# Performance work log

Measured on AMD Instinct MI355X. Metric: run time of the kernel, lower is better.

## Reference

```python
import jax, jax.numpy as jnp
import numpy as np

B, S, E, H = 4, 1024, 512, 16

def setup_inputs() -> dict:
    key = jax.random.key(0)
    ks = jax.random.split(key, 6)
    return {
        "x": jax.random.normal(ks[0], (B, S, E), dtype=jnp.float32),
        "Wq": jax.random.normal(ks[1], (E, E), dtype=jnp.float32) * (E ** -0.5),
        "Wk": jax.random.normal(ks[2], (E, E), dtype=jnp.float32) * (E ** -0.5),
        "Wv": jax.random.normal(ks[3], (E, E), dtype=jnp.float32) * (E ** -0.5),
        "W1": jax.random.normal(ks[4], (H, 2 * E), dtype=jnp.float32) * ((2 * E) ** -0.5),
        "b1": jnp.zeros((H,), dtype=jnp.float32),
        "W2": jax.random.normal(ks[5], (1, H), dtype=jnp.float32) * (H ** -0.5),
        "b2": jnp.zeros((1,), dtype=jnp.float32),
    }

def reference(x, Wq, Wk, Wv, W1, b1, W2, b2):
    embed_dim = x.shape[-1]
    # nn.Linear: y = x @ W.T
    Q = jnp.einsum('bse,oe->bso', x, Wq)
    K = jnp.einsum('bse,oe->bso', x, Wk)
    V = jnp.einsum('bse,oe->bso', x, Wv)
    scores = jnp.einsum('bqe,bke->bqk', Q, K) / jnp.sqrt(jnp.float32(embed_dim))
    # Estimator on concat([Q_i, K_j]): split W1 so we never materialize the
    # [B,S,S,2E] pair tensor; concat(q,k)@W1.T == q@W1[:, :E].T + k@W1[:, E:].T
    W1q, W1k = W1[:, :embed_dim], W1[:, embed_dim:]
    hq = jnp.einsum('bqe,he->bqh', Q, W1q)          # [B,S,H]
    hk = jnp.einsum('bke,he->bkh', K, W1k)          # [B,S,H]
    hid = jnp.tanh(hq[:, :, None, :] + hk[:, None, :, :] + b1)  # [B,S,S,H]
    est = jnp.einsum('bqkh,h->bqk', hid, W2[0]) + b2[0]
    attn = jax.nn.softmax(scores + est, axis=-1)
    return jnp.einsum('bqk,bke->bqe', attn, V)
```

## Files before the change

### kernel.cpp

```cpp
#include <hip/hip_runtime.h>
#include <hip/hip_fp16.h>


#define DEVI __device__ __forceinline__

typedef _Float16 half8 __attribute__((ext_vector_type(8)));
typedef _Float16 half4v __attribute__((ext_vector_type(4)));
typedef float f32x4 __attribute__((ext_vector_type(4)));

DEVI void gload16(const void* g, void* l) {
  __builtin_amdgcn_global_load_lds(
      (const __attribute__((address_space(1))) void*)g,
      (__attribute__((address_space(3))) void*)l, 16, 0, 0);
}

DEVI half8 cvt8(float4 a, float4 b) {
  half8 h;
  h[0] = (_Float16)a.x; h[1] = (_Float16)a.y; h[2] = (_Float16)a.z; h[3] = (_Float16)a.w;
  h[4] = (_Float16)b.x; h[5] = (_Float16)b.y; h[6] = (_Float16)b.z; h[7] = (_Float16)b.w;
  return h;
}

#define MEMBAR asm volatile("" ::: "memory")
#define LGKM0  asm volatile("s_waitcnt lgkmcnt(0)" ::: "memory")
#define SBAR   __builtin_amdgcn_s_barrier()
#define VMW(n) asm volatile("s_waitcnt vmcnt(" #n ")" ::: "memory")

__global__ __launch_bounds__(256) void k_qkv(
    const float* __restrict__ x, const float* __restrict__ Wq,
    const float* __restrict__ Wk, const float* __restrict__ Wv,
    _Float16* __restrict__ Qh, _Float16* __restrict__ Kh, _Float16* __restrict__ Vt)
{
  __shared__ _Float16 As[2 * 128 * 32], Bs[2 * 64 * 32];
  const int bid0 = blockIdx.x;
  const int bid = (bid0 & 7) * 96 + (bid0 >> 3);
  const int mt = bid / 24, ntg = bid - mt * 24;
  const int mat = ntg >> 3, ntl = ntg & 7;
  const float* W = (mat == 0) ? Wq : ((mat == 1) ? Wk : Wv);
  const float* Ag = x + (size_t)mt * 128 * 512;
  const float* Bg = W + (size_t)ntl * 64 * 512;

  const int tid = threadIdx.x;
  const int l = tid & 63, w = tid >> 6, wr = w >> 1, wc = w & 1;
  const int frow = l & 15, kof = (l >> 4) * 8;
  const int ar = tid >> 1, ac = (tid & 1) * 16;
  const int br = tid >> 2, bc = (tid & 3) * 8;

  f32x4 acc[4][2] = {};
  float4 fa0, fa1, fa2, fa3, fb0, fb1;

  auto loadT = [&](int kt) {
    const float4* pa = (const float4*)(Ag + (size_t)ar * 512 + kt + ac);
    fa0 = pa[0]; fa1 = pa[1]; fa2 = pa[2]; fa3 = pa[3];
    const float4* pb = (const float4*)(Bg + (size_t)br * 512 + kt + bc);
    fb0 = pb[0]; fb1 = pb[1];
  };
  auto writeT = [&](int buf) {
    *(half8*)(As + buf * 4096 + ar * 32 + ac)     = cvt8(fa0, fa1);
    *(half8*)(As + buf * 4096 + ar * 32 + ac + 8) = cvt8(fa2, fa3);
    *(half8*)(Bs + buf * 2048 + br * 32 + bc)     = cvt8(fb0, fb1);
  };
  auto compute = [&](int buf) {
    half8 aF[4], bF[2];
#pragma unroll
    for (int mf = 0; mf < 4; ++mf)
      aF[mf] = *(const half8*)(As + buf * 4096 + (wr * 64 + mf * 16 + frow) * 32 + kof);
#pragma unroll
    for (int nf = 0; nf < 2; ++nf)
      bF[nf] = *(const half8*)(Bs + buf * 2048 + (wc * 32 + nf * 16 + frow) * 32 + kof);
#pragma unroll
    for (int mf = 0; mf < 4; ++mf)
#pragma unroll
      for (int nf = 0; nf < 2; ++nf)
        acc[mf][nf] = __builtin_amdgcn_mfma_f32_16x16x32_f16(aF[mf], bF[nf], acc[mf][nf], 0, 0, 0);
  };

  loadT(0); writeT(0);
  __syncthreads();
  int cur = 0;
  for (int kt = 32; kt < 512; kt += 32) {
    loadT(kt);
    compute(cur);
    writeT(cur ^ 1);
    __syncthreads();
    cur ^= 1;
  }
  compute(cur);

  const int nc0 = ntl * 64 + wc * 32 + frow;
  const int mr0 = mt * 128 + wr * 64 + (l >> 4) * 4;
#pragma unroll
  for (int mf = 0; mf < 4; ++mf)
#pragma unroll
    for (int nf = 0; nf < 2; ++nf) {
      const int col = nc0 + nf * 16;
      if (mat == 0) {
#pragma unroll
        for (int r = 0; r < 4; ++r)
          Qh[(size_t)(mr0 + mf * 16 + r) * 512 + col] = (_Float16)acc[mf][nf][r];
      } else if (mat == 1) {
#pragma unroll
        for (int r = 0; r < 4; ++r)
          Kh[(size_t)(mr0 + mf * 16 + r) * 512 + col] = (_Float16)acc[mf][nf][r];
      } else {
        const int row0 = mr0 + mf * 16;
        const int bb = row0 >> 10, s0 = row0 & 1023;
        half4v hv;
#pragma unroll
        for (int r = 0; r < 4; ++r) hv[r] = (_Float16)acc[mf][nf][r];
        *(half4v*)(Vt + ((size_t)bb * 512 + col) * 1024 + s0) = hv;
      }
    }
}

__global__ __launch_bounds__(256) void k_scores(
    const _Float16* __restrict__ Qh, const _Float16* __restrict__ Kh,
    const float* __restrict__ W1, const float* __restrict__ b1,
    const float* __restrict__ W2,
    _Float16* __restrict__ P, float* __restrict__ partials)
{
  __shared__ _Float16 As[3 * 128 * 32];
  __shared__ _Float16 Bs[3 * 64 * 32];
  __shared__ _Float16 W1fq[16 * 512], W1fk[16 * 512];
  __shared__ float w2s[16];
  float* Eqs = (float*)As;
  float* Eks = ((float*)As) + 128 * 17;
  float* sums = (float*)Bs;

  const int kt = blockIdx.x, qt = blockIdx.y, b = blockIdx.z;
  const int tid = threadIdx.x;
  const int l = tid & 63, w = tid >> 6, wr = w >> 1, wc = w & 1;
  const int frow = l & 15, kof = (l >> 4) * 8;
  if (tid < 16) w2s[tid] = W2[tid];

#pragma unroll
  for (int c = tid; c < 1024; c += 256) {
    const int t = c >> 6, lj = c & 63;
    const int e0 = t * 32 + (lj >> 4) * 8;
    const float4* pq = (const float4*)(W1 + (lj & 15) * 1024 + e0);
    *(half8*)(W1fq + c * 8) = cvt8(pq[0], pq[1]);
    const float4* pk = (const float4*)(W1 + (lj & 15) * 1024 + 512 + e0);
    *(half8*)(W1fk + c * 8) = cvt8(pk[0], pk[1]);
  }

  const _Float16* Ag = Qh + (size_t)(b * 1024 + qt * 128) * 512;
  const _Float16* Bg = Kh + (size_t)(b * 1024 + kt * 64) * 512;
  const int srA = tid >> 2, scA = (tid & 3) * 8;

  f32x4 acc[4][2] = {};
  f32x4 hqA[4] = {};
  f32x4 hkA[2] = {};

  auto stage = [&](int buf, int k2) {
    gload16(Ag + (size_t)srA * 512 + k2 + scA,        As + buf * 4096 + tid * 8);
    gload16(Ag + (size_t)(srA + 64) * 512 + k2 + scA, As + buf * 4096 + (tid + 256) * 8);
    gload16(Bg + (size_t)srA * 512 + k2 + scA,        Bs + buf * 2048 + tid * 8);
  };
  auto compute = [&](int buf, int tstep) {
    half8 aF[4], bF[2];
#pragma unroll
    for (int mf = 0; mf < 4; ++mf)
      aF[mf] = *(const half8*)(As + buf * 4096 + (wr * 64 + mf * 16 + frow) * 32 + kof);
#pragma unroll
    for (int nf = 0; nf < 2; ++nf)
      bF[nf] = *(const half8*)(Bs + buf * 2048 + (wc * 32 + nf * 16 + frow) * 32 + kof);
    const half8 wqF = *(const half8*)(W1fq + tstep * 512 + l * 8);
    const half8 wkF = *(const half8*)(W1fk + tstep * 512 + l * 8);
#pragma unroll
    for (int mf = 0; mf < 4; ++mf)
#pragma unroll
      for (int nf = 0; nf < 2; ++nf)
        acc[mf][nf] = __builtin_amdgcn_mfma_f32_16x16x32_f16(aF[mf], bF[nf], acc[mf][nf], 0, 0, 0);
#pragma unroll
    for (int mf = 0; mf < 4; ++mf)
      hqA[mf] = __builtin_amdgcn_mfma_f32_16x16x32_f16(aF[mf], wqF, hqA[mf], 0, 0, 0);
#pragma unroll
    for (int nf = 0; nf < 2; ++nf)
      hkA[nf] = __builtin_amdgcn_mfma_f32_16x16x32_f16(wkF, bF[nf], hkA[nf], 0, 0, 0);
  };

  stage(0, 0); stage(1, 32); stage(2, 64);
  LGKM0;
  for (int t = 0; t < 13; ++t) {
    VMW(6); SBAR; MEMBAR;
    compute(t % 3, t);
    MEMBAR; SBAR;
    stage(t % 3, 32 * (t + 3));
  }
  VMW(6); SBAR; MEMBAR; compute(1, 13); MEMBAR; SBAR;
  VMW(3); SBAR; MEMBAR; compute(2, 14); MEMBAR; SBAR;
  VMW(0); SBAR; MEMBAR; compute(0, 15);
  MEMBAR; SBAR;

  const int lr0 = wr * 64 + (l >> 4) * 4;
  if (wc == 0) {
    const float b1v = b1[frow];
#pragma unroll
    for (int mf = 0; mf < 4; ++mf)
#pragma unroll
      for (int r = 0; r < 4; ++r)
        Eqs[(lr0 + mf * 16 + r) * 17 + frow] = __expf(2.f * (hqA[mf][r] + b1v));
  }
  if (wr == 0) {
#pragma unroll
    for (int nf = 0; nf < 2; ++nf)
#pragma unroll
      for (int r = 0; r < 4; ++r)
        Eks[(wc * 32 + nf * 16 + frow) * 17 + ((l >> 4) * 4 + r)] = __expf(2.f * hkA[nf][r]);
  }
  __syncthreads();

  const float scale = 0.044194173824159216f;
#pragma unroll
  for (int mf = 0; mf < 4; ++mf)
#pragma unroll
    for (int nf = 0; nf < 2; ++nf)
      acc[mf][nf] *= scale;

  const int lc0 = wc * 32 + frow;
  float w2sum = 0.f;
#pragma unroll
  for (int h = 0; h < 16; ++h) {
    const float w2v = w2s[h];
    const float tw2 = -2.f * w2v;
    w2sum += w2v;
    float Eb[2];
#pragma unroll
    for (int nf = 0; nf < 2; ++nf) Eb[nf] = Eks[(lc0 + nf * 16) * 17 + h];
#pragma unroll
    for (int mf = 0; mf < 4; ++mf)
#pragma unroll
      for (int r = 0; r < 4; ++r) {
        const float Ea = Eqs[(lr0 + mf * 16 + r) * 17 + h];
#pragma unroll
        for (int nf = 0; nf < 2; ++nf) {
          const float t = __builtin_fmaf(Ea, Eb[nf], 1.f);
          const float rc = __builtin_amdgcn_rcpf(t);
          acc[mf][nf][r] = __builtin_fmaf(tw2, rc, acc[mf][nf][r]);
        }
      }
  }

  const float bias = w2sum - 6.f;
#pragma unroll
  for (int mf = 0; mf < 4; ++mf)
#pragma unroll
    for (int nf = 0; nf < 2; ++nf)
#pragma unroll
      for (int r = 0; r < 4; ++r)
        acc[mf][nf][r] = __expf(acc[mf][nf][r] + bias);

  float rp[4][4];
#pragma unroll
  for (int mf = 0; mf < 4; ++mf)
#pragma unroll
    for (int r = 0; r < 4; ++r) {
      float s = acc[mf][0][r] + acc[mf][1][r];
#pragma unroll
      for (int off = 1; off < 16; off <<= 1) s += __shfl_xor(s, off);
      rp[mf][r] = s;
    }

  __syncthreads();
  if (frow == 0) {
#pragma unroll
    for (int mf = 0; mf < 4; ++mf)
#pragma unroll
      for (int r = 0; r < 4; ++r)
        sums[wc * 128 + lr0 + mf * 16 + r] = rp[mf][r];
  }
  __syncthreads();
  if (tid < 128)
    partials[((size_t)b * 1024 + qt * 128 + tid) * 16 + kt] = sums[tid] + sums[128 + tid];

  _Float16* Pb = P + ((size_t)b << 20);
#pragma unroll
  for (int mf = 0; mf < 4; ++mf)
#pragma unroll
    for (int nf = 0; nf < 2; ++nf) {
      const int col = kt * 64 + lc0 + nf * 16;
#pragma unroll
      for (int r = 0; r < 4; ++r)
        Pb[(size_t)(qt * 128 + lr0 + mf * 16 + r) * 1024 + col] = (_Float16)acc[mf][nf][r];
    }
}

__global__ __launch_bounds__(256) void k_pv(
    const _Float16* __restrict__ P, const _Float16* __restrict__ Vt,
    const float* __restrict__ partials, float* __restrict__ out)
{
  __shared__ _Float16 As[3 * 64 * 32], Bs[3 * 64 * 32];
  __shared__ float rinv[64];
  const int nt = blockIdx.x, mt = blockIdx.y, b = blockIdx.z;
  const int tid = threadIdx.x;
  if (tid < 64) {
    const float4* pp = (const float4*)(partials + ((size_t)b * 1024 + mt * 64 + tid) * 16);
    float4 s0 = pp[0], s1 = pp[1], s2 = pp[2], s3 = pp[3];
    rinv[tid] = 1.f / (((s0.x + s0.y + s0.z + s0.w) + (s1.x + s1.y + s1.z + s1.w)) +
                       ((s2.x + s2.y + s2.z + s2.w) + (s3.x + s3.y + s3.z + s3.w)));
  }

  const int l = tid & 63, w = tid >> 6, wr = w >> 1, wc = w & 1;
  const int frow = l & 15, kof = (l >> 4) * 8;
  const int srow = tid >> 2, scol = (tid & 3) * 8;
  const _Float16* Ag = P + ((size_t)b << 20) + (size_t)mt * 64 * 1024 + (size_t)srow * 1024 + scol;
  const _Float16* Bg = Vt + ((size_t)b * 512 + nt * 64) * 1024 + (size_t)srow * 1024 + scol;

  f32x4 acc[2][2] = {};

  auto stage = [&](int buf, int kt2) {
    gload16(Ag + kt2, As + buf * 2048 + tid * 8);
    gload16(Bg + kt2, Bs + buf * 2048 + tid * 8);
  };
  auto compute = [&](int buf) {
    half8 aF[2], bF[2];
#pragma unroll
    for (int mf = 0; mf < 2; ++mf)
      aF[mf] = *(const half8*)(As + buf * 2048 + (wr * 32 + mf * 16 + frow) * 32 + kof);
#pragma unroll
    for (int nf = 0; nf < 2; ++nf)
      bF[nf] = *(const half8*)(Bs + buf * 2048 + (wc * 32 + nf * 16 + frow) * 32 + kof);
#pragma unroll
    for (int mf = 0; mf < 2; ++mf)
#pragma unroll
      for (int nf = 0; nf < 2; ++nf)
        acc[mf][nf] = __builtin_amdgcn_mfma_f32_16x16x32_f16(aF[mf], bF[nf], acc[mf][nf], 0, 0, 0);
  };

  stage(0, 0); stage(1, 32); stage(2, 64);
  LGKM0;
  for (int t = 0; t < 29; ++t) {
    VMW(4); SBAR; MEMBAR;
    compute(t % 3);
    MEMBAR; SBAR;
    stage(t % 3, 32 * (t + 3));
  }
  VMW(4); SBAR; MEMBAR; compute(2); MEMBAR; SBAR;
  VMW(2); SBAR; MEMBAR; compute(0); MEMBAR; SBAR;
  VMW(0); SBAR; MEMBAR; compute(1);

  const int lr0 = wr * 32 + (l >> 4) * 4, lc0 = wc * 32 + frow;
#pragma unroll
  for (int mf = 0; mf < 2; ++mf)
#pragma unroll
    for (int nf = 0; nf < 2; ++nf) {
      const int col = nt * 64 + lc0 + nf * 16;
#pragma unroll
      for (int r = 0; r < 4; ++r) {
        const int lrow = lr0 + mf * 16 + r;
        out[((size_t)(b * 1024 + mt * 64 + lrow)) * 512 + col] = acc[mf][nf][r] * rinv[lrow];
      }
    }
}

extern "C" void kernel_launch(void* const* d_in, const int* in_sizes, int n_in,
                              void* d_out, int out_size, void* d_ws, size_t ws_size,
                              hipStream_t stream)
{
  const float* x  = (const float*)d_in[0];
  const float* Wq = (const float*)d_in[1];
  const float* Wk = (const float*)d_in[2];
  const float* Wv = (const float*)d_in[3];
  const float* W1 = (const float*)d_in[4];
  const float* b1 = (const float*)d_in[5];
  const float* W2 = (const float*)d_in[6];
  float* out = (float*)d_out;

  char* ws = (char*)d_ws;
  size_t off = 0;
  auto alloc = [&](size_t bytes) { char* p = ws + off; off += (bytes + 255) & ~255ull; return p; };
  _Float16* Qh    = (_Float16*)alloc(4096ull * 512 * 2);
  _Float16* Kh    = (_Float16*)alloc(4096ull * 512 * 2);
  _Float16* Vt    = (_Float16*)alloc(4ull * 512 * 1024 * 2);
  float*  parts   = (float*)alloc(4096ull * 16 * 4);
  _Float16* P     = (_Float16*)alloc(4ull * 1024 * 1024 * 2);

  k_qkv<<<768, 256, 0, stream>>>(x, Wq, Wk, Wv, Qh, Kh, Vt);
  k_scores<<<dim3(16, 8, 4), 256, 0, stream>>>(Qh, Kh, W1, b1, W2, P, parts);
  k_pv<<<dim3(8, 16, 4), 256, 0, stream>>>(P, Vt, parts, out);
}
```

Before: 65.43 us.

## Pad QKV GEMM LDS rows and deepen register prefetch to two tiles

The QKV projection GEMM pads its LDS tile rows from 32 to 40 halves to cut bank conflicts on fragment reads. It also switches to two register staging sets, so global loads for tile t+2 are in flight while tile t is computed, and replaces __syncthreads with explicit lgkmcnt waits plus barriers. In exchange it uses more registers and LDS, and the loop is hard-coded to the K=512 trip count.

```diff
diff --git a/kernel.cpp b/kernel.cpp
--- a/kernel.cpp
+++ b/kernel.cpp
@@ -31,7 +31,7 @@
     const float* __restrict__ Wk, const float* __restrict__ Wv,
     _Float16* __restrict__ Qh, _Float16* __restrict__ Kh, _Float16* __restrict__ Vt)
 {
-  __shared__ _Float16 As[2 * 128 * 32], Bs[2 * 64 * 32];
+  __shared__ _Float16 As[2 * 128 * 40], Bs[2 * 64 * 40];
   const int bid0 = blockIdx.x;
   const int bid = (bid0 & 7) * 96 + (bid0 >> 3);
   const int mt = bid / 24, ntg = bid - mt * 24;
@@ -47,27 +47,39 @@
   const int br = tid >> 2, bc = (tid & 3) * 8;
 
   f32x4 acc[4][2] = {};
-  float4 fa0, fa1, fa2, fa3, fb0, fb1;
-
-  auto loadT = [&](int kt) {
+  float4 a0, a1, a2, a3, a4, a5;
+  float4 b0, b1, b2, b3, b4, b5;
+
+  auto loadA = [&](int kt) {
     const float4* pa = (const float4*)(Ag + (size_t)ar * 512 + kt + ac);
-    fa0 = pa[0]; fa1 = pa[1]; fa2 = pa[2]; fa3 = pa[3];
+    a0 = pa[0]; a1 = pa[1]; a2 = pa[2]; a3 = pa[3];
     const float4* pb = (const float4*)(Bg + (size_t)br * 512 + kt + bc);
-    fb0 = pb[0]; fb1 = pb[1];
-  };
-  auto writeT = [&](int buf) {
-    *(half8*)(As + buf * 4096 + ar * 32 + ac)     = cvt8(fa0, fa1);
-    *(half8*)(As + buf * 4096 + ar * 32 + ac + 8) = cvt8(fa2, fa3);
-    *(half8*)(Bs + buf * 2048 + br * 32 + bc)     = cvt8(fb0, fb1);
+    a4 = pb[0]; a5 = pb[1];
+  };
+  auto loadB = [&](int kt) {
+    const float4* pa = (const float4*)(Ag + (size_t)ar * 512 + kt + ac);
+    b0 = pa[0]; b1 = pa[1]; b2 = pa[2]; b3 = pa[3];
+    const float4* pb = (const float4*)(Bg + (size_t)br * 512 + kt + bc);
+    b4 = pb[0]; b5 = pb[1];
+  };
+  auto writeA = [&](int buf) {
+    *(half8*)(As + buf * 5120 + ar * 40 + ac)     = cvt8(a0, a1);
+    *(half8*)(As + buf * 5120 + ar * 40 + ac + 8) = cvt8(a2, a3);
+    *(half8*)(Bs + buf * 2560 + br * 40 + bc)     = cvt8(a4, a5);
+  };
+  auto writeB = [&](int buf) {
+    *(half8*)(As + buf * 5120 + ar * 40 + ac)     = cvt8(b0, b1);
+    *(half8*)(As + buf * 5120 + ar * 40 + ac + 8) = cvt8(b2, b3);
+    *(half8*)(Bs + buf * 2560 + br * 40 + bc)     = cvt8(b4, b5);
   };
   auto compute = [&](int buf) {
     half8 aF[4], bF[2];
 #pragma unroll
     for (int mf = 0; mf < 4; ++mf)
-      aF[mf] = *(const half8*)(As + buf * 4096 + (wr * 64 + mf * 16 + frow) * 32 + kof);
-#pragma unroll
-    for (int nf = 0; nf < 2; ++nf)
-      bF[nf] = *(const half8*)(Bs + buf * 2048 + (wc * 32 + nf * 16 + frow) * 32 + kof);
+      aF[mf] = *(const half8*)(As + buf * 5120 + (wr * 64 + mf * 16 + frow) * 40 + kof);
+#pragma unroll
+    for (int nf = 0; nf < 2; ++nf)
+      bF[nf] = *(const half8*)(Bs + buf * 2560 + (wc * 32 + nf * 16 + frow) * 40 + kof);
 #pragma unroll
     for (int mf = 0; mf < 4; ++mf)
 #pragma unroll
@@ -75,17 +87,23 @@
         acc[mf][nf] = __builtin_amdgcn_mfma_f32_16x16x32_f16(aF[mf], bF[nf], acc[mf][nf], 0, 0, 0);
   };
 
-  loadT(0); writeT(0);
-  __syncthreads();
-  int cur = 0;
-  for (int kt = 32; kt < 512; kt += 32) {
-    loadT(kt);
-    compute(cur);
-    writeT(cur ^ 1);
-    __syncthreads();
-    cur ^= 1;
-  }
-  compute(cur);
+  loadA(0); writeA(0);
+  loadB(32);
+  LGKM0; SBAR; MEMBAR;
+  for (int t = 0; t < 14; t += 2) {
+    compute(0);
+    loadA(32 * (t + 2));
+    writeB(1);
+    LGKM0; SBAR; MEMBAR;
+    compute(1);
+    loadB(32 * (t + 3));
+    writeA(0);
+    LGKM0; SBAR; MEMBAR;
+  }
+  compute(0);
+  writeB(1);
+  LGKM0; SBAR; MEMBAR;
+  compute(1);
 
   const int nc0 = ntl * 64 + wc * 32 + frow;
   const int mr0 = mt * 128 + wr * 64 + (l >> 4) * 4;
```

Measured after the change: 67.67 us. +3.4%, slower.

## Fuse Q/K/V projections into one 128x192 tile per block and pack fp16 conversions

Applied to the files above, without the earlier changes.

The QKV projection kernel now gives each block a 128-row tile of x against 64 columns of each of Wq, Wk and Wv together, a 192-wide B tile. This cuts the grid from 768 to 256 blocks and reads and converts each x tile once instead of three times. The float-to-half conversion now uses packed round-toward-zero conversion instructions. The trade-offs are more accumulator registers (24 MFMA tiles per wave), a larger LDS footprint, and fewer blocks, which may lower occupancy and parallelism on a 256-CU device. Rounding toward zero also differs slightly from the previous round-to-nearest conversion.

```diff
diff --git a/kernel.cpp b/kernel.cpp
--- a/kernel.cpp
+++ b/kernel.cpp
@@ -6,6 +6,7 @@
 
 typedef _Float16 half8 __attribute__((ext_vector_type(8)));
 typedef _Float16 half4v __attribute__((ext_vector_type(4)));
+typedef __fp16 fp16x2 __attribute__((ext_vector_type(2)));
 typedef float f32x4 __attribute__((ext_vector_type(4)));
 
 DEVI void gload16(const void* g, void* l) {
@@ -21,6 +22,19 @@
   return h;
 }
 
+DEVI half8 cvt8pk(float4 a, float4 b) {
+  fp16x2 h0 = __builtin_amdgcn_cvt_pkrtz(a.x, a.y);
+  fp16x2 h1 = __builtin_amdgcn_cvt_pkrtz(a.z, a.w);
+  fp16x2 h2 = __builtin_amdgcn_cvt_pkrtz(b.x, b.y);
+  fp16x2 h3 = __builtin_amdgcn_cvt_pkrtz(b.z, b.w);
+  half8 h;
+  h[0] = (_Float16)h0[0]; h[1] = (_Float16)h0[1];
+  h[2] = (_Float16)h1[0]; h[3] = (_Float16)h1[1];
+  h[4] = (_Float16)h2[0]; h[5] = (_Float16)h2[1];
+  h[6] = (_Float16)h3[0]; h[7] = (_Float16)h3[1];
+  return h;
+}
+
 #define MEMBAR asm volatile("" ::: "memory")
 #define LGKM0  asm volatile("s_waitcnt lgkmcnt(0)" ::: "memory")
 #define SBAR   __builtin_amdgcn_s_barrier()
@@ -31,47 +45,71 @@
     const float* __restrict__ Wk, const float* __restrict__ Wv,
     _Float16* __restrict__ Qh, _Float16* __restrict__ Kh, _Float16* __restrict__ Vt)
 {
-  __shared__ _Float16 As[2 * 128 * 32], Bs[2 * 64 * 32];
+  __shared__ _Float16 As[2 * 128 * 32];
+  __shared__ _Float16 Bs[2 * 192 * 32];
   const int bid0 = blockIdx.x;
-  const int bid = (bid0 & 7) * 96 + (bid0 >> 3);
-  const int mt = bid / 24, ntg = bid - mt * 24;
-  const int mat = ntg >> 3, ntl = ntg & 7;
-  const float* W = (mat == 0) ? Wq : ((mat == 1) ? Wk : Wv);
-  const float* Ag = x + (size_t)mt * 128 * 512;
-  const float* Bg = W + (size_t)ntl * 64 * 512;
+  const int bid = (bid0 & 7) * 32 + (bid0 >> 3);
+  const int mt = bid >> 3, cg = bid & 7;
+  const int cbase = cg * 64;
 
   const int tid = threadIdx.x;
   const int l = tid & 63, w = tid >> 6, wr = w >> 1, wc = w & 1;
   const int frow = l & 15, kof = (l >> 4) * 8;
-  const int ar = tid >> 1, ac = (tid & 1) * 16;
-  const int br = tid >> 2, bc = (tid & 3) * 8;
-
-  f32x4 acc[4][2] = {};
-  float4 fa0, fa1, fa2, fa3, fb0, fb1;
+
+  const float* pA[2];
+  int aOff[2];
+#pragma unroll
+  for (int i = 0; i < 2; ++i) {
+    const int p = i * 256 + tid, row = p >> 2, cp = p & 3;
+    pA[i] = x + (size_t)(mt * 128 + row) * 512 + cp * 8;
+    aOff[i] = row * 32 + cp * 8;
+  }
+  const float* pB[3];
+  int bOff[3];
+#pragma unroll
+  for (int i = 0; i < 3; ++i) {
+    const int p = i * 256 + tid, row = p >> 2, cp = p & 3;
+    const int matv = row >> 6, wrow = cbase + (row & 63);
+    const float* W = (matv == 0) ? Wq : ((matv == 1) ? Wk : Wv);
+    pB[i] = W + (size_t)wrow * 512 + cp * 8;
+    bOff[i] = row * 32 + cp * 8;
+  }
+
+  f32x4 acc[4][6] = {};
+  float4 ra[2][2], rb[3][2];
 
   auto loadT = [&](int kt) {
-    const float4* pa = (const float4*)(Ag + (size_t)ar * 512 + kt + ac);
-    fa0 = pa[0]; fa1 = pa[1]; fa2 = pa[2]; fa3 = pa[3];
-    const float4* pb = (const float4*)(Bg + (size_t)br * 512 + kt + bc);
-    fb0 = pb[0]; fb1 = pb[1];
+#pragma unroll
+    for (int i = 0; i < 2; ++i) {
+      const float4* p = (const float4*)(pA[i] + kt);
+      ra[i][0] = p[0]; ra[i][1] = p[1];
+    }
+#pragma unroll
+    for (int i = 0; i < 3; ++i) {
+      const float4* p = (const float4*)(pB[i] + kt);
+      rb[i][0] = p[0]; rb[i][1] = p[1];
+    }
   };
   auto writeT = [&](int buf) {
-    *(half8*)(As + buf * 4096 + ar * 32 + ac)     = cvt8(fa0, fa1);
-    *(half8*)(As + buf * 4096 + ar * 32 + ac + 8) = cvt8(fa2, fa3);
-    *(half8*)(Bs + buf * 2048 + br * 32 + bc)     = cvt8(fb0, fb1);
+#pragma unroll
+    for (int i = 0; i < 2; ++i)
+      *(half8*)(As + buf * 4096 + aOff[i]) = cvt8pk(ra[i][0], ra[i][1]);
+#pragma unroll
+    for (int i = 0; i < 3; ++i)
+      *(half8*)(Bs + buf * 6144 + bOff[i]) = cvt8pk(rb[i][0], rb[i][1]);
   };
   auto compute = [&](int buf) {
-    half8 aF[4], bF[2];
+    half8 aF[4], bF[6];
 #pragma unroll
     for (int mf = 0; mf < 4; ++mf)
       aF[mf] = *(const half8*)(As + buf * 4096 + (wr * 64 + mf * 16 + frow) * 32 + kof);
 #pragma unroll
-    for (int nf = 0; nf < 2; ++nf)
-      bF[nf] = *(const half8*)(Bs + buf * 2048 + (wc * 32 + nf * 16 + frow) * 32 + kof);
-#pragma unroll
-    for (int mf = 0; mf < 4; ++mf)
-#pragma unroll
-      for (int nf = 0; nf < 2; ++nf)
+    for (int nf = 0; nf < 6; ++nf)
+      bF[nf] = *(const half8*)(Bs + buf * 6144 + (wc * 96 + nf * 16 + frow) * 32 + kof);
+#pragma unroll
+    for (int mf = 0; mf < 4; ++mf)
+#pragma unroll
+      for (int nf = 0; nf < 6; ++nf)
         acc[mf][nf] = __builtin_amdgcn_mfma_f32_16x16x32_f16(aF[mf], bF[nf], acc[mf][nf], 0, 0, 0);
   };
 
@@ -87,18 +125,19 @@
   }
   compute(cur);
 
-  const int nc0 = ntl * 64 + wc * 32 + frow;
   const int mr0 = mt * 128 + wr * 64 + (l >> 4) * 4;
 #pragma unroll
   for (int mf = 0; mf < 4; ++mf)
 #pragma unroll
-    for (int nf = 0; nf < 2; ++nf) {
-      const int col = nc0 + nf * 16;
-      if (mat == 0) {
+    for (int nf = 0; nf < 6; ++nf) {
+      const int gcol = wc * 96 + nf * 16 + frow;
+      const int matv = gcol >> 6;
+      const int col = cbase + (gcol & 63);
+      if (matv == 0) {
 #pragma unroll
         for (int r = 0; r < 4; ++r)
           Qh[(size_t)(mr0 + mf * 16 + r) * 512 + col] = (_Float16)acc[mf][nf][r];
-      } else if (mat == 1) {
+      } else if (matv == 1) {
 #pragma unroll
         for (int r = 0; r < 4; ++r)
           Kh[(size_t)(mr0 + mf * 16 + r) * 512 + col] = (_Float16)acc[mf][nf][r];
@@ -375,7 +414,7 @@
   float*  parts   = (float*)alloc(4096ull * 16 * 4);
   _Float16* P     = (_Float16*)alloc(4ull * 1024 * 1024 * 2);
 
-  k_qkv<<<768, 256, 0, stream>>>(x, Wq, Wk, Wv, Qh, Kh, Vt);
+  k_qkv<<<256, 256, 0, stream>>>(x, Wq, Wk, Wv, Qh, Kh, Vt);
   k_scores<<<dim3(16, 8, 4), 256, 0, stream>>>(Qh, Kh, W1, b1, W2, P, parts);
   k_pv<<<dim3(8, 16, 4), 256, 0, stream>>>(P, Vt, parts, out);
 }
```

After: 65.88 us. Within noise of the previous version (+0.7%).
